# Kernel optimization log

Hardware: AMD Instinct MI355X
Metric: run time of the kernel (lower is better)

The kernel has to match this reference:

```python
import jax, jax.numpy as jnp
import numpy as np


def setup_inputs() -> dict:
    key = jax.random.key(0)
    k1, k2 = jax.random.split(key)
    x = jax.random.normal(k1, (128, 128, 256), dtype=jnp.float32)
    embed = jax.random.normal(k2, (16384, 256), dtype=jnp.float32)
    return {"x": x, "embed": embed}


BETA = 0.25


def reference(x, embed):
    dim = embed.shape[1]
    n_embed = embed.shape[0]
    latent = x.reshape(-1, dim)  # [N, d]
    # squared euclidean distance: ||z||^2 - 2 z.e^T + ||e||^2  -> [N, K]
    dist = (
        jnp.sum(latent * latent, axis=1, keepdims=True)
        - 2.0 * jnp.einsum("nd,kd->nk", latent, embed)
        + jnp.sum(embed * embed, axis=1)[None, :]
    )
    embed_ind = jnp.argmax(-dist, axis=1)  # [N]
    # one-hot histogram of code usage (segment_sum == onehot.sum(0))
    embed_onehot_sum = jax.ops.segment_sum(
        jnp.ones_like(embed_ind, dtype=jnp.int32), embed_ind, num_segments=n_embed
    )
    unused_codes = jnp.sum(embed_onehot_sum == 0)
    x_q = embed[embed_ind].reshape(x.shape)
    quant_loss = jnp.mean((x_q - jax.lax.stop_gradient(x)) ** 2) + BETA * jnp.mean(
        (x - jax.lax.stop_gradient(x_q)) ** 2
    )
    # straight-through estimator
    x_q = x + jax.lax.stop_gradient(x_q - x)
    embed_ind = embed_ind.reshape(x.shape[:-1])
    return (x_q, quant_loss, unused_codes, embed_ind)
```

## Files before the change

kernel.cpp:

```cpp
#include <hip/hip_runtime.h>

#define N_LAT 16384
#define N_EMB 16384
#define DIM   256
#define XQ_ELEMS (N_LAT * DIM)

typedef __attribute__((ext_vector_type(8))) _Float16 f16x8;
typedef __attribute__((ext_vector_type(4))) float    f32x4;

#define SWZ(a) ((a) ^ ((((a) >> 6) & 7) << 4))

#define GLD16(g, l) __builtin_amdgcn_global_load_lds( \
    (const __attribute__((address_space(1))) unsigned int*)(g), \
    (__attribute__((address_space(3))) unsigned int*)(l), 16, 0, 0)


__global__ __launch_bounds__(256) void k_convert(const float* __restrict__ src,
                                                 char* __restrict__ hi,
                                                 char* __restrict__ lo) {
    const int gid = blockIdx.x * 256 + threadIdx.x;
    const int row = gid >> 5, k8 = gid & 31;
    const float* s = src + (size_t)row * DIM + k8 * 8;
    float f[8];
    *reinterpret_cast<float4*>(&f[0]) = *reinterpret_cast<const float4*>(s);
    *reinterpret_cast<float4*>(&f[4]) = *reinterpret_cast<const float4*>(s + 4);
    f16x8 hv, lv;
#pragma unroll
    for (int m = 0; m < 8; ++m) {
        const _Float16 h = (_Float16)f[m];
        hv[m] = h;
        lv[m] = (_Float16)(f[m] - (float)h);
    }
    const int dst = ((row >> 7) * 8 + (k8 >> 2)) * 8192 + SWZ((row & 127) * 64 + (k8 & 3) * 16);
    *reinterpret_cast<f16x8*>(hi + dst) = hv;
    *reinterpret_cast<f16x8*>(lo + dst) = lv;
}

__global__ __launch_bounds__(256) void k_enorm(const float* __restrict__ embed,
                                               float* __restrict__ enorm) {
    const int gid  = blockIdx.x * 256 + threadIdx.x;
    const int wave = gid >> 6;
    const int lane = threadIdx.x & 63;
    for (int row = wave; row < N_EMB; row += 1024) {
        const float4 v = *reinterpret_cast<const float4*>(&embed[row * DIM + lane * 4]);
        double s = (double)v.x * v.x + (double)v.y * v.y +
                   (double)v.z * v.z + (double)v.w * v.w;
#pragma unroll
        for (int m = 32; m; m >>= 1) s += __shfl_xor(s, m, 64);
        if (lane == 0) enorm[row] = (float)s;
    }
}

__global__ __launch_bounds__(256) void k_argmin(const char* __restrict__ xhi,
                                                const char* __restrict__ xlo,
                                                const char* __restrict__ ehi,
                                                const char* __restrict__ elo,
                                                const float* __restrict__ enorm,
                                                unsigned long long* __restrict__ best) {
    __shared__ char smem[32768];
    char* As_hi = smem;
    char* As_lo = smem + 8192;
    char* Bs_hi = smem + 16384;
    char* Bs_lo = smem + 24576;

    const int tid = threadIdx.x;
    const int w   = tid >> 6;
    const int l   = tid & 63;
    const int lg  = l >> 4;
    const int lr  = l & 15;

    const int row0 = blockIdx.x * 128;
    const int kc   = blockIdx.y;

    const size_t abase = (size_t)blockIdx.x * 8 * 8192 + (size_t)w * 2048;
    const int    lo16  = l * 16;

    int aoff[2];
#pragma unroll
    for (int i = 0; i < 2; ++i) {
        const int r = w * 32 + i * 16 + lr;
        aoff[i] = SWZ(r * 64 + lg * 16);
    }
    int boff[8];
#pragma unroll
    for (int j = 0; j < 8; ++j) {
        const int c = j * 16 + lr;
        boff[j] = SWZ(c * 64 + lg * 16);
    }

    unsigned long long pmin[2][4];
#pragma unroll
    for (int i = 0; i < 2; ++i)
#pragma unroll
        for (int t = 0; t < 4; ++t) pmin[i][t] = ~0ULL;

    for (int ct = 0; ct < 8; ++ct) {
        const int    cb    = kc * 8 + ct;
        const size_t bbase = (size_t)cb * 8 * 8192 + (size_t)w * 2048;

        f32x4 acc[2][8];
#pragma unroll
        for (int i = 0; i < 2; ++i)
#pragma unroll
            for (int j = 0; j < 8; ++j) acc[i][j] = (f32x4)0.0f;

        for (int ks = 0; ks < 8; ++ks) {
            __syncthreads();
#pragma unroll
            for (int q = 0; q < 2; ++q) {
                const int    o  = w * 2048 + q * 1024;
                const size_t ga = abase + (size_t)ks * 8192 + q * 1024 + lo16;
                const size_t gb = bbase + (size_t)ks * 8192 + q * 1024 + lo16;
                GLD16(xhi + ga, As_hi + o);
                GLD16(xlo + ga, As_lo + o);
                GLD16(ehi + gb, Bs_hi + o);
                GLD16(elo + gb, Bs_lo + o);
            }
            __syncthreads();

            f16x8 ah[2], al[2];
#pragma unroll
            for (int i = 0; i < 2; ++i) {
                ah[i] = *reinterpret_cast<const f16x8*>(As_hi + aoff[i]);
                al[i] = *reinterpret_cast<const f16x8*>(As_lo + aoff[i]);
            }
#pragma unroll
            for (int j = 0; j < 8; ++j) {
                const f16x8 bh = *reinterpret_cast<const f16x8*>(Bs_hi + boff[j]);
                const f16x8 bl = *reinterpret_cast<const f16x8*>(Bs_lo + boff[j]);
#pragma unroll
                for (int i = 0; i < 2; ++i) {
                    acc[i][j] = __builtin_amdgcn_mfma_f32_16x16x32_f16(ah[i], bh, acc[i][j], 0, 0, 0);
                    acc[i][j] = __builtin_amdgcn_mfma_f32_16x16x32_f16(ah[i], bl, acc[i][j], 0, 0, 0);
                    acc[i][j] = __builtin_amdgcn_mfma_f32_16x16x32_f16(al[i], bh, acc[i][j], 0, 0, 0);
                }
            }
        }
        const int colbase = kc * 1024 + ct * 128;
#pragma unroll
        for (int j = 0; j < 8; ++j) {
            const int   col = colbase + j * 16 + lr;
            const float s   = enorm[col];
#pragma unroll
            for (int i = 0; i < 2; ++i)
#pragma unroll
                for (int t = 0; t < 4; ++t) {
                    const float v = fmaf(-2.0f, acc[i][j][t], s);
                    unsigned u = __float_as_uint(v);
                    u = (u & 0x80000000u) ? ~u : (u | 0x80000000u);
                    const unsigned long long p = ((unsigned long long)u << 32) | (unsigned)col;
                    if (p < pmin[i][t]) pmin[i][t] = p;
                }
        }
    }
#pragma unroll
    for (int i = 0; i < 2; ++i)
#pragma unroll
        for (int t = 0; t < 4; ++t) {
            unsigned long long p = pmin[i][t];
#pragma unroll
            for (int m = 1; m < 16; m <<= 1) {
                const unsigned long long q = __shfl_xor(p, m, 64);
                if (q < p) p = q;
            }
            if (lr == 0) {
                const int row = row0 + w * 32 + i * 16 + lg * 4 + t;
                atomicMin(&best[row], p);
            }
        }
}

__global__ __launch_bounds__(256) void k_gather(const float* __restrict__ x,
                                                const float* __restrict__ embed,
                                                const unsigned long long* __restrict__ best,
                                                float* __restrict__ out,
                                                int* __restrict__ hist,
                                                double* __restrict__ bsum) {
    __shared__ double partial[4];
    const int row = blockIdx.x;
    const int t   = threadIdx.x;
    const int idx = (int)(best[row] & 0xFFFFFFFFULL);
    const float e  = embed[(size_t)idx * DIM + t];
    const float xv = x[(size_t)row * DIM + t];
    const float d  = e - xv;
    out[(size_t)row * DIM + t] = xv + d;
    double sq = (double)d * (double)d;
#pragma unroll
    for (int m = 32; m; m >>= 1) sq += __shfl_xor(sq, m, 64);
    const int lane = t & 63, wv = t >> 6;
    if (lane == 0) partial[wv] = sq;
    __syncthreads();
    if (t == 0) {
        bsum[row] = partial[0] + partial[1] + partial[2] + partial[3];
        atomicAdd(&hist[idx], 1);
        out[XQ_ELEMS + 2 + row] = (float)idx;
    }
}

__global__ __launch_bounds__(256) void k_final(const int* __restrict__ hist,
                                               const double* __restrict__ bsum,
                                               float* __restrict__ out) {
    __shared__ int    cpart[4];
    __shared__ double spart[4];
    const int t = threadIdx.x;
    int cnt = 0; double s = 0.0;
    for (int i = t; i < N_EMB; i += 256) {
        cnt += (hist[i] == 0) ? 1 : 0;
        s += bsum[i];
    }
#pragma unroll
    for (int m = 32; m; m >>= 1) {
        cnt += __shfl_xor(cnt, m, 64);
        s   += __shfl_xor(s, m, 64);
    }
    const int lane = t & 63, wv = t >> 6;
    if (lane == 0) { cpart[wv] = cnt; spart[wv] = s; }
    __syncthreads();
    if (t == 0) {
        const double sse = spart[0] + spart[1] + spart[2] + spart[3];
        out[XQ_ELEMS + 0] = (float)(1.25 * sse / (double)XQ_ELEMS);
        out[XQ_ELEMS + 1] = (float)(cpart[0] + cpart[1] + cpart[2] + cpart[3]);
    }
}

extern "C" void kernel_launch(void* const* d_in, const int* in_sizes, int n_in,
                              void* d_out, int out_size, void* d_ws, size_t ws_size,
                              hipStream_t stream) {
    const float* x     = (const float*)d_in[0];
    const float* embed = (const float*)d_in[1];
    float* out = (float*)d_out;

    char* ws = (char*)d_ws;
    float*              enorm = (float*)(ws + 0);
    unsigned long long* best  = (unsigned long long*)(ws + 65536);
    int*                hist  = (int*)(ws + 196608);
    double*             bsum  = (double*)(ws + 262144);
    char*               xhi   = ws + 393216;
    char*               xlo   = xhi + 8388608;
    char*               ehi   = xlo + 8388608;
    char*               elo   = ehi + 8388608;

    hipMemsetAsync(best, 0xFF, N_LAT * sizeof(unsigned long long), stream);
    hipMemsetAsync(hist, 0x00, N_EMB * sizeof(int), stream);

    k_convert<<<2048, 256, 0, stream>>>(x, xhi, xlo);
    k_convert<<<2048, 256, 0, stream>>>(embed, ehi, elo);
    k_enorm  <<<256, 256, 0, stream>>>(embed, enorm);
    k_argmin <<<dim3(128, 16), 256, 0, stream>>>(xhi, xlo, ehi, elo, enorm, best);
    k_gather <<<N_LAT, 256, 0, stream>>>(x, embed, best, out, hist, bsum);
    k_final  <<<1, 256, 0, stream>>>(hist, bsum, out);
}
```

Baseline: 525.2 us.

## Double-buffer LDS tiles in argmin GEMM and fuse embed norm into convert

```diff
diff --git a/kernel.cpp b/kernel.cpp
--- a/kernel.cpp
+++ b/kernel.cpp
@@ -17,7 +17,8 @@
 
 __global__ __launch_bounds__(256) void k_convert(const float* __restrict__ src,
                                                  char* __restrict__ hi,
-                                                 char* __restrict__ lo) {
+                                                 char* __restrict__ lo,
+                                                 float* __restrict__ norm) {
     const int gid = blockIdx.x * 256 + threadIdx.x;
     const int row = gid >> 5, k8 = gid & 31;
     const float* s = src + (size_t)row * DIM + k8 * 8;
@@ -25,29 +26,21 @@
     *reinterpret_cast<float4*>(&f[0]) = *reinterpret_cast<const float4*>(s);
     *reinterpret_cast<float4*>(&f[4]) = *reinterpret_cast<const float4*>(s + 4);
     f16x8 hv, lv;
+    double nrm = 0.0;
 #pragma unroll
     for (int m = 0; m < 8; ++m) {
         const _Float16 h = (_Float16)f[m];
         hv[m] = h;
         lv[m] = (_Float16)(f[m] - (float)h);
+        nrm += (double)f[m] * (double)f[m];
     }
     const int dst = ((row >> 7) * 8 + (k8 >> 2)) * 8192 + SWZ((row & 127) * 64 + (k8 & 3) * 16);
     *reinterpret_cast<f16x8*>(hi + dst) = hv;
     *reinterpret_cast<f16x8*>(lo + dst) = lv;
-}
-
-__global__ __launch_bounds__(256) void k_enorm(const float* __restrict__ embed,
-                                               float* __restrict__ enorm) {
-    const int gid  = blockIdx.x * 256 + threadIdx.x;
-    const int wave = gid >> 6;
-    const int lane = threadIdx.x & 63;
-    for (int row = wave; row < N_EMB; row += 1024) {
-        const float4 v = *reinterpret_cast<const float4*>(&embed[row * DIM + lane * 4]);
-        double s = (double)v.x * v.x + (double)v.y * v.y +
-                   (double)v.z * v.z + (double)v.w * v.w;
-#pragma unroll
-        for (int m = 32; m; m >>= 1) s += __shfl_xor(s, m, 64);
-        if (lane == 0) enorm[row] = (float)s;
+    if (norm) {
+#pragma unroll
+        for (int m = 16; m; m >>= 1) nrm += __shfl_xor(nrm, m, 64);
+        if (k8 == 0) norm[row] = (float)nrm;
     }
 }
 
@@ -57,11 +50,8 @@
                                                 const char* __restrict__ elo,
                                                 const float* __restrict__ enorm,
                                                 unsigned long long* __restrict__ best) {
-    __shared__ char smem[32768];
-    char* As_hi = smem;
-    char* As_lo = smem + 8192;
-    char* Bs_hi = smem + 16384;
-    char* Bs_lo = smem + 24576;
+    __shared__ char smem[65536];
+    char* const sm = smem;
 
     const int tid = threadIdx.x;
     const int w   = tid >> 6;
@@ -72,21 +62,31 @@
     const int row0 = blockIdx.x * 128;
     const int kc   = blockIdx.y;
 
-    const size_t abase = (size_t)blockIdx.x * 8 * 8192 + (size_t)w * 2048;
-    const int    lo16  = l * 16;
+    const size_t lane16 = (size_t)(w * 2048 + l * 16);
+    const size_t gA  = (size_t)blockIdx.x * 65536 + lane16;
+    const size_t gB0 = (size_t)kc * 8 * 65536 + lane16;
+
+    auto STAGE = [&](int ct_, int ks_, int half) {
+        const int    o  = half * 32768 + w * 2048;
+        const size_t ga = gA + (size_t)ks_ * 8192;
+        const size_t gb = gB0 + (size_t)ct_ * 65536 + (size_t)ks_ * 8192;
+#pragma unroll
+        for (int q = 0; q < 2; ++q) {
+            GLD16(xhi + ga + q * 1024, sm + o +         q * 1024);
+            GLD16(xlo + ga + q * 1024, sm + o +  8192 + q * 1024);
+            GLD16(ehi + gb + q * 1024, sm + o + 16384 + q * 1024);
+            GLD16(elo + gb + q * 1024, sm + o + 24576 + q * 1024);
+        }
+    };
 
     int aoff[2];
 #pragma unroll
-    for (int i = 0; i < 2; ++i) {
-        const int r = w * 32 + i * 16 + lr;
-        aoff[i] = SWZ(r * 64 + lg * 16);
-    }
+    for (int i = 0; i < 2; ++i)
+        aoff[i] = SWZ((w * 32 + i * 16 + lr) * 64 + lg * 16);
     int boff[8];
 #pragma unroll
-    for (int j = 0; j < 8; ++j) {
-        const int c = j * 16 + lr;
-        boff[j] = SWZ(c * 64 + lg * 16);
-    }
+    for (int j = 0; j < 8; ++j)
+        boff[j] = SWZ((j * 16 + lr) * 64 + lg * 16);
 
     unsigned long long pmin[2][4];
 #pragma unroll
@@ -94,10 +94,11 @@
 #pragma unroll
         for (int t = 0; t < 4; ++t) pmin[i][t] = ~0ULL;
 
+    STAGE(0, 0, 0);
+    __syncthreads();
+    int half = 0;
+
     for (int ct = 0; ct < 8; ++ct) {
-        const int    cb    = kc * 8 + ct;
-        const size_t bbase = (size_t)cb * 8 * 8192 + (size_t)w * 2048;
-
         f32x4 acc[2][8];
 #pragma unroll
         for (int i = 0; i < 2; ++i)
@@ -105,29 +106,21 @@
             for (int j = 0; j < 8; ++j) acc[i][j] = (f32x4)0.0f;
 
         for (int ks = 0; ks < 8; ++ks) {
-            __syncthreads();
-#pragma unroll
-            for (int q = 0; q < 2; ++q) {
-                const int    o  = w * 2048 + q * 1024;
-                const size_t ga = abase + (size_t)ks * 8192 + q * 1024 + lo16;
-                const size_t gb = bbase + (size_t)ks * 8192 + q * 1024 + lo16;
-                GLD16(xhi + ga, As_hi + o);
-                GLD16(xlo + ga, As_lo + o);
-                GLD16(ehi + gb, Bs_hi + o);
-                GLD16(elo + gb, Bs_lo + o);
-            }
-            __syncthreads();
-
+            int nks = ks + 1, nct = ct;
+            if (nks == 8) { nks = 0; ++nct; }
+            if (nct < 8) STAGE(nct, nks, half ^ 1);
+
+            const int hb = half * 32768;
             f16x8 ah[2], al[2];
 #pragma unroll
             for (int i = 0; i < 2; ++i) {
-                ah[i] = *reinterpret_cast<const f16x8*>(As_hi + aoff[i]);
-                al[i] = *reinterpret_cast<const f16x8*>(As_lo + aoff[i]);
+                ah[i] = *reinterpret_cast<const f16x8*>(sm + hb +        aoff[i]);
+                al[i] = *reinterpret_cast<const f16x8*>(sm + hb + 8192 + aoff[i]);
             }
 #pragma unroll
             for (int j = 0; j < 8; ++j) {
-                const f16x8 bh = *reinterpret_cast<const f16x8*>(Bs_hi + boff[j]);
-                const f16x8 bl = *reinterpret_cast<const f16x8*>(Bs_lo + boff[j]);
+                const f16x8 bh = *reinterpret_cast<const f16x8*>(sm + hb + 16384 + boff[j]);
+                const f16x8 bl = *reinterpret_cast<const f16x8*>(sm + hb + 24576 + boff[j]);
 #pragma unroll
                 for (int i = 0; i < 2; ++i) {
                     acc[i][j] = __builtin_amdgcn_mfma_f32_16x16x32_f16(ah[i], bh, acc[i][j], 0, 0, 0);
@@ -135,6 +128,8 @@
                     acc[i][j] = __builtin_amdgcn_mfma_f32_16x16x32_f16(al[i], bh, acc[i][j], 0, 0, 0);
                 }
             }
+            __syncthreads();
+            half ^= 1;
         }
         const int colbase = kc * 1024 + ct * 128;
 #pragma unroll
@@ -243,9 +238,8 @@
     hipMemsetAsync(best, 0xFF, N_LAT * sizeof(unsigned long long), stream);
     hipMemsetAsync(hist, 0x00, N_EMB * sizeof(int), stream);
 
-    k_convert<<<2048, 256, 0, stream>>>(x, xhi, xlo);
-    k_convert<<<2048, 256, 0, stream>>>(embed, ehi, elo);
-    k_enorm  <<<256, 256, 0, stream>>>(embed, enorm);
+    k_convert<<<2048, 256, 0, stream>>>(x, xhi, xlo, nullptr);
+    k_convert<<<2048, 256, 0, stream>>>(embed, ehi, elo, enorm);
     k_argmin <<<dim3(128, 16), 256, 0, stream>>>(xhi, xlo, ehi, elo, enorm, best);
     k_gather <<<N_LAT, 256, 0, stream>>>(x, embed, best, out, hist, bsum);
     k_final  <<<1, 256, 0, stream>>>(hist, bsum, out);
```

New measurement: 563.2 us. +7.2%, slower.
